# Performance work log

Measured on AMD Instinct MI355X. Metric: run time of the kernel, lower is better.

The kernel has to match this reference:

```python
import jax, jax.numpy as jnp
import numpy as np

B, L = 32768, 2048
NG, GL = 4, 64  # n_groups (bag channels), group length (MIL feature dim)


def _wn(v, g):
    # weight_norm: w = g * v / ||v|| (norm over in_ch, kernel dims per out channel)
    nrm = jnp.sqrt(jnp.sum(v * v, axis=(1, 2), keepdims=True))
    return g[:, None, None] * v / nrm


def _conv1d(x, w, b):
    # x: (N, C, L), w: (O, I, K), padding=1, stride=1
    out = jax.lax.conv_general_dilated(
        x, w, window_strides=(1,), padding=[(1, 1)],
        dimension_numbers=('NCH', 'OIH', 'NCH'))
    return out + b[None, :, None]


def setup_inputs() -> dict:
    key = jax.random.key(0)
    ks = jax.random.split(key, 12)
    x = jax.random.normal(ks[0], (B, L, 1), dtype=jnp.float32)
    index_all = jax.random.randint(ks[1], (NG, GL), 0, L)
    # conv1 (1 -> 1, k=3) with weight_norm params
    v1 = 0.01 * jax.random.normal(ks[2], (1, 1, 3), dtype=jnp.float32)
    g1 = jnp.ones((1,), dtype=jnp.float32)
    b1 = jnp.zeros((1,), dtype=jnp.float32)
    # conv2 (4 -> 4, k=3) with weight_norm params
    v2 = 0.01 * jax.random.normal(ks[3], (NG, NG, 3), dtype=jnp.float32)
    g2 = jnp.ones((NG,), dtype=jnp.float32)
    b2 = jnp.zeros((NG,), dtype=jnp.float32)
    # IMILmask linears (64 -> 64)
    sc = 1.0 / np.sqrt(GL)
    W1 = sc * jax.random.normal(ks[4], (GL, GL), dtype=jnp.float32)
    bl1 = jnp.zeros((GL,), dtype=jnp.float32)
    W2 = sc * jax.random.normal(ks[5], (GL, GL), dtype=jnp.float32)
    bl2 = jnp.zeros((GL,), dtype=jnp.float32)
    Wa = sc * jax.random.normal(ks[6], (GL, GL), dtype=jnp.float32)
    ba = jnp.zeros((GL,), dtype=jnp.float32)
    return {"x": x, "index_all": index_all, "v1": v1, "g1": g1, "b1": b1,
            "v2": v2, "g2": g2, "b2": b2, "W1": W1, "bl1": bl1,
            "W2": W2, "bl2": bl2, "Wa": Wa, "ba": ba}


def reference(x, index_all, v1, g1, b1, v2, g2, b2, W1, bl1, W2, bl2, Wa, ba):
    xp = jnp.transpose(x, (0, 2, 1))  # (B, 1, L)
    # site branch: conv -> tanh (in net) -> tanh again (forward applies tanh1 twice)
    w1 = _wn(v1, g1)
    x_site = jnp.tanh(jnp.tanh(_conv1d(xp, w1, b1)))  # (B, 1, L)
    # mapping_converge: ragged gather into bags; original detaches x here
    xg = jax.lax.stop_gradient(xp)[:, 0, :]           # (B, L)
    xm = xg[:, index_all]                             # (B, NG, GL)
    # IMILmask
    l1 = jax.nn.relu(xm @ W1.T + bl1)
    l2 = jax.nn.relu(xm @ W2.T + bl2)
    A = jax.nn.sigmoid((l1 + l2) @ Wa.T + ba)
    xmask = (A + 1.0) * xm                            # (B, NG, GL)
    # bag branch conv (channels = NG, length = GL)
    w2 = _wn(v2, g2)
    x_bag = jnp.tanh(jnp.tanh(_conv1d(xmask, w2, b2)))
    return (x_bag, x_site)
```

## Files before the change

kernel.cpp:

```cpp
#include <hip/hip_runtime.h>
#include <cmath>

#define BATCH 32768
#define LEN   2048
#define NGRP  4
#define GLEN  64

__device__ __forceinline__ float fast_tanh(float x){
    float ax = fabsf(x);
    float e  = __expf(-2.f*ax);
    float r  = __fdividef(1.f - e, 1.f + e);
    return copysignf(r, x);
}
__device__ __forceinline__ float tanh2(float x){ return fast_tanh(fast_tanh(x)); }

__global__ __launch_bounds__(256) void k_site(
    const float* __restrict__ x, const int* __restrict__ idx,
    const float* __restrict__ v1, const float* __restrict__ g1, const float* __restrict__ b1,
    float* __restrict__ xsite, float* __restrict__ xmws, int use_ws)
{
    float nrm = sqrtf(v1[0]*v1[0] + v1[1]*v1[1] + v1[2]*v1[2]);
    float s  = g1[0]/nrm;
    float w0 = v1[0]*s, w1 = v1[1]*s, w2 = v1[2]*s, bb = b1[0];

    __shared__ int sidx[256];
    sidx[threadIdx.x] = idx[threadIdx.x];
    __syncthreads();

    const int t = threadIdx.x;
    for (int rr = 0; rr < 4; ++rr){
        const int row = blockIdx.x*4 + rr;
        const float* xr  = x     + (size_t)row*LEN;
        float*       orr = xsite + (size_t)row*LEN;
        const int p0 = t*8;
        float4 a = *(const float4*)(xr + p0);
        float4 b = *(const float4*)(xr + p0 + 4);
        if (use_ws)
            xmws[(size_t)row*256 + t] = xr[sidx[t]];
        float in[10];
        in[0] = (p0 == 0) ? 0.f : xr[p0-1];
        in[1]=a.x; in[2]=a.y; in[3]=a.z; in[4]=a.w;
        in[5]=b.x; in[6]=b.y; in[7]=b.z; in[8]=b.w;
        in[9] = (p0 + 8 >= LEN) ? 0.f : xr[p0+8];
        float o[8];
        #pragma unroll
        for (int c = 0; c < 8; ++c)
            o[c] = tanh2(fmaf(w0, in[c], fmaf(w1, in[c+1], fmaf(w2, in[c+2], bb))));
        *(float4*)(orr + p0)     = make_float4(o[0],o[1],o[2],o[3]);
        *(float4*)(orr + p0 + 4) = make_float4(o[4],o[5],o[6],o[7]);
    }
}

__global__ __launch_bounds__(128) void k_bag(
    const float* __restrict__ x, const float* __restrict__ xmws, const int* __restrict__ idx,
    const float* __restrict__ v2, const float* __restrict__ g2, const float* __restrict__ b2,
    const float* __restrict__ W1, const float* __restrict__ bl1,
    const float* __restrict__ W2, const float* __restrict__ bl2,
    const float* __restrict__ Wa, const float* __restrict__ ba,
    float* __restrict__ xbag, int use_ws)
{
    const int lane = threadIdx.x & 63;
    const int wave = threadIdx.x >> 6;
    const int rl   = lane >> 2;
    const int g    = lane & 3;
    const int row  = blockIdx.x*32 + wave*16 + rl;

    float xm[GLEN];
    if (use_ws){
        const float4* p = (const float4*)(xmws + (size_t)row*256 + g*64);
        #pragma unroll
        for (int q = 0; q < 16; ++q){
            float4 v = p[q];
            xm[4*q+0]=v.x; xm[4*q+1]=v.y; xm[4*q+2]=v.z; xm[4*q+3]=v.w;
        }
    } else {
        const float* xr = x + (size_t)row*LEN;
        #pragma unroll
        for (int k = 0; k < GLEN; ++k) xm[k] = xr[idx[g*64 + k]];
    }

    float l12[GLEN];
    const float4* W1v = (const float4*)W1;
    const float4* W2v = (const float4*)W2;
    #pragma unroll 2
    for (int j = 0; j < GLEN; ++j){
        float a1 = bl1[j], a2 = bl2[j];
        #pragma unroll
        for (int q = 0; q < 16; ++q){
            float4 u = W1v[j*16 + q];
            float4 w = W2v[j*16 + q];
            a1 = fmaf(xm[4*q+0],u.x, fmaf(xm[4*q+1],u.y, fmaf(xm[4*q+2],u.z, fmaf(xm[4*q+3],u.w, a1))));
            a2 = fmaf(xm[4*q+0],w.x, fmaf(xm[4*q+1],w.y, fmaf(xm[4*q+2],w.z, fmaf(xm[4*q+3],w.w, a2))));
        }
        l12[j] = fmaxf(a1, 0.f) + fmaxf(a2, 0.f);
    }

    const float4* Wav = (const float4*)Wa;
    #pragma unroll 2
    for (int j = 0; j < GLEN; ++j){
        float a = ba[j];
        #pragma unroll
        for (int q = 0; q < 16; ++q){
            float4 u = Wav[j*16 + q];
            a = fmaf(l12[4*q+0],u.x, fmaf(l12[4*q+1],u.y, fmaf(l12[4*q+2],u.z, fmaf(l12[4*q+3],u.w, a))));
        }
        float A = __fdividef(1.f, 1.f + __expf(-a));
        xm[j] = (A + 1.f) * xm[j];
    }

    __shared__ float X[2*16*260];
    float* Xw = X + wave*(16*260) + rl*260 + g*65;
    #pragma unroll
    for (int k = 0; k < GLEN; ++k) Xw[k] = xm[k];
    __syncthreads();

    float wv[NGRP][3];
    float nn = 0.f;
    #pragma unroll
    for (int i = 0; i < NGRP; ++i)
        #pragma unroll
        for (int d = 0; d < 3; ++d){ float tv = v2[(g*NGRP + i)*3 + d]; nn += tv*tv; }
    float sc = g2[g] / sqrtf(nn);
    #pragma unroll
    for (int i = 0; i < NGRP; ++i)
        #pragma unroll
        for (int d = 0; d < 3; ++d) wv[i][d] = v2[(g*NGRP + i)*3 + d] * sc;

    float acc[GLEN];
    const float bo = b2[g];
    #pragma unroll
    for (int j = 0; j < GLEN; ++j) acc[j] = bo;
    const float* Xr = X + wave*(16*260) + rl*260;
    #pragma unroll
    for (int i = 0; i < NGRP; ++i){
        const float* c = Xr + i*65;
        float xp_ = 0.f, xc = c[0];
        #pragma unroll
        for (int j = 0; j < GLEN; ++j){
            float xn = (j < GLEN-1) ? c[j+1] : 0.f;
            acc[j] = fmaf(wv[i][0], xp_, fmaf(wv[i][1], xc, fmaf(wv[i][2], xn, acc[j])));
            xp_ = xc; xc = xn;
        }
    }

    float* ob = xbag + ((size_t)row*NGRP + g)*GLEN;
    #pragma unroll
    for (int q = 0; q < 16; ++q){
        float4 v = make_float4(tanh2(acc[4*q+0]), tanh2(acc[4*q+1]),
                               tanh2(acc[4*q+2]), tanh2(acc[4*q+3]));
        *(float4*)(ob + 4*q) = v;
    }
}

extern "C" void kernel_launch(void* const* d_in, const int* in_sizes, int n_in,
                              void* d_out, int out_size, void* d_ws, size_t ws_size,
                              hipStream_t stream) {
    const float* x   = (const float*)d_in[0];
    const int*   idx = (const int*)  d_in[1];
    const float* v1  = (const float*)d_in[2];
    const float* g1  = (const float*)d_in[3];
    const float* b1  = (const float*)d_in[4];
    const float* v2  = (const float*)d_in[5];
    const float* g2  = (const float*)d_in[6];
    const float* b2  = (const float*)d_in[7];
    const float* W1  = (const float*)d_in[8];
    const float* bl1 = (const float*)d_in[9];
    const float* W2  = (const float*)d_in[10];
    const float* bl2 = (const float*)d_in[11];
    const float* Wa  = (const float*)d_in[12];
    const float* ba  = (const float*)d_in[13];

    float* xbag  = (float*)d_out;
    float* xsite = (float*)d_out + (size_t)BATCH*NGRP*GLEN;
    float* xmws  = (float*)d_ws;
    const int use_ws = (ws_size >= (size_t)BATCH*256*sizeof(float)) ? 1 : 0;

    k_site<<<BATCH/4, 256, 0, stream>>>(x, idx, v1, g1, b1, xsite, xmws, use_ws);
    k_bag <<<BATCH/32, 128, 0, stream>>>(x, xmws, idx, v2, g2, b2,
                                         W1, bl1, W2, bl2, Wa, ba, xbag, use_ws);
}
```

Measured before the change: 710.6 us.

## Split bag MLP outputs across four threads per group via shared memory staging

k_bag now uses 256 threads per block, with four threads per (row, group). Each thread computes 16 of the 64 output features for the two linears, the attention layer and the conv, and intermediates are exchanged through padded shared memory. Results are staged in LDS so the final xbag store is contiguous and coalesced per block. The aim is to cut the per-thread register arrays of 64 floats, raise occupancy and coalesce the output. The cost is more syncthreads, more LDS traffic, and each thread still loading the full 64-element xm row, so that read is duplicated four times.

```diff
diff --git a/kernel.cpp b/kernel.cpp
--- a/kernel.cpp
+++ b/kernel.cpp
@@ -51,7 +51,7 @@
     }
 }
 
-__global__ __launch_bounds__(128) void k_bag(
+__global__ __launch_bounds__(256, 4) void k_bag(
     const float* __restrict__ x, const float* __restrict__ xmws, const int* __restrict__ idx,
     const float* __restrict__ v2, const float* __restrict__ g2, const float* __restrict__ b2,
     const float* __restrict__ W1, const float* __restrict__ bl1,
@@ -59,15 +59,20 @@
     const float* __restrict__ Wa, const float* __restrict__ ba,
     float* __restrict__ xbag, int use_ws)
 {
-    const int lane = threadIdx.x & 63;
-    const int wave = threadIdx.x >> 6;
-    const int rl   = lane >> 2;
-    const int g    = lane & 3;
-    const int row  = blockIdx.x*32 + wave*16 + rl;
+    const int t  = threadIdx.x;
+    const int s  = t & 3;
+    const int g  = (t >> 2) & 3;
+    const int rl = t >> 4;
+    const int row = blockIdx.x*16 + rl;
+    const int rg  = (rl << 2) | g;
+    const int j0  = s << 4;
+
+    __shared__ float b1s[64*65];
+    __shared__ float b2s[64*65];
 
     float xm[GLEN];
     if (use_ws){
-        const float4* p = (const float4*)(xmws + (size_t)row*256 + g*64);
+        const float4* p = (const float4*)(xmws + (size_t)row*256 + (g << 6));
         #pragma unroll
         for (int q = 0; q < 16; ++q){
             float4 v = p[q];
@@ -76,79 +81,113 @@
     } else {
         const float* xr = x + (size_t)row*LEN;
         #pragma unroll
-        for (int k = 0; k < GLEN; ++k) xm[k] = xr[idx[g*64 + k]];
-    }
-
-    float l12[GLEN];
-    const float4* W1v = (const float4*)W1;
-    const float4* W2v = (const float4*)W2;
-    #pragma unroll 2
-    for (int j = 0; j < GLEN; ++j){
-        float a1 = bl1[j], a2 = bl2[j];
-        #pragma unroll
+        for (int k = 0; k < GLEN; ++k) xm[k] = xr[idx[(g << 6) + k]];
+    }
+
+    {
+        const float4* W1v = (const float4*)W1;
+        const float4* W2v = (const float4*)W2;
+        float* Lw = b1s + rg*65 + j0;
+        #pragma unroll 2
+        for (int jj = 0; jj < 16; ++jj){
+            const int j = j0 + jj;
+            float a1 = bl1[j], a2 = bl2[j];
+            #pragma unroll
+            for (int q = 0; q < 16; ++q){
+                float4 u = W1v[j*16 + q];
+                float4 w = W2v[j*16 + q];
+                a1 = fmaf(xm[4*q+0],u.x, fmaf(xm[4*q+1],u.y, fmaf(xm[4*q+2],u.z, fmaf(xm[4*q+3],u.w, a1))));
+                a2 = fmaf(xm[4*q+0],w.x, fmaf(xm[4*q+1],w.y, fmaf(xm[4*q+2],w.z, fmaf(xm[4*q+3],w.w, a2))));
+            }
+            Lw[jj] = fmaxf(a1, 0.f) + fmaxf(a2, 0.f);
+        }
+    }
+    __syncthreads();
+
+    float acc[16];
+    #pragma unroll
+    for (int jj = 0; jj < 16; ++jj) acc[jj] = ba[j0 + jj];
+    {
+        const float4* Wav = (const float4*)Wa;
+        const float* Lr = b1s + rg*65;
+        #pragma unroll 2
         for (int q = 0; q < 16; ++q){
-            float4 u = W1v[j*16 + q];
-            float4 w = W2v[j*16 + q];
-            a1 = fmaf(xm[4*q+0],u.x, fmaf(xm[4*q+1],u.y, fmaf(xm[4*q+2],u.z, fmaf(xm[4*q+3],u.w, a1))));
-            a2 = fmaf(xm[4*q+0],w.x, fmaf(xm[4*q+1],w.y, fmaf(xm[4*q+2],w.z, fmaf(xm[4*q+3],w.w, a2))));
-        }
-        l12[j] = fmaxf(a1, 0.f) + fmaxf(a2, 0.f);
-    }
-
-    const float4* Wav = (const float4*)Wa;
-    #pragma unroll 2
-    for (int j = 0; j < GLEN; ++j){
-        float a = ba[j];
-        #pragma unroll
-        for (int q = 0; q < 16; ++q){
-            float4 u = Wav[j*16 + q];
-            a = fmaf(l12[4*q+0],u.x, fmaf(l12[4*q+1],u.y, fmaf(l12[4*q+2],u.z, fmaf(l12[4*q+3],u.w, a))));
-        }
-        float A = __fdividef(1.f, 1.f + __expf(-a));
-        xm[j] = (A + 1.f) * xm[j];
-    }
-
-    __shared__ float X[2*16*260];
-    float* Xw = X + wave*(16*260) + rl*260 + g*65;
-    #pragma unroll
-    for (int k = 0; k < GLEN; ++k) Xw[k] = xm[k];
-    __syncthreads();
-
-    float wv[NGRP][3];
-    float nn = 0.f;
-    #pragma unroll
-    for (int i = 0; i < NGRP; ++i)
-        #pragma unroll
-        for (int d = 0; d < 3; ++d){ float tv = v2[(g*NGRP + i)*3 + d]; nn += tv*tv; }
-    float sc = g2[g] / sqrtf(nn);
-    #pragma unroll
-    for (int i = 0; i < NGRP; ++i)
-        #pragma unroll
-        for (int d = 0; d < 3; ++d) wv[i][d] = v2[(g*NGRP + i)*3 + d] * sc;
-
-    float acc[GLEN];
-    const float bo = b2[g];
-    #pragma unroll
-    for (int j = 0; j < GLEN; ++j) acc[j] = bo;
-    const float* Xr = X + wave*(16*260) + rl*260;
-    #pragma unroll
-    for (int i = 0; i < NGRP; ++i){
-        const float* c = Xr + i*65;
-        float xp_ = 0.f, xc = c[0];
-        #pragma unroll
-        for (int j = 0; j < GLEN; ++j){
-            float xn = (j < GLEN-1) ? c[j+1] : 0.f;
-            acc[j] = fmaf(wv[i][0], xp_, fmaf(wv[i][1], xc, fmaf(wv[i][2], xn, acc[j])));
-            xp_ = xc; xc = xn;
-        }
-    }
-
-    float* ob = xbag + ((size_t)row*NGRP + g)*GLEN;
-    #pragma unroll
-    for (int q = 0; q < 16; ++q){
-        float4 v = make_float4(tanh2(acc[4*q+0]), tanh2(acc[4*q+1]),
-                               tanh2(acc[4*q+2]), tanh2(acc[4*q+3]));
-        *(float4*)(ob + 4*q) = v;
+            const float l0 = Lr[4*q+0], l1 = Lr[4*q+1], l2 = Lr[4*q+2], l3 = Lr[4*q+3];
+            #pragma unroll
+            for (int jj = 0; jj < 16; ++jj){
+                float4 u = Wav[(j0+jj)*16 + q];
+                acc[jj] = fmaf(l0,u.x, fmaf(l1,u.y, fmaf(l2,u.z, fmaf(l3,u.w, acc[jj]))));
+            }
+        }
+    }
+
+    {
+        float xs[16];
+        if (use_ws){
+            const float4* p = (const float4*)(xmws + (size_t)row*256 + (g << 6) + j0);
+            #pragma unroll
+            for (int c = 0; c < 4; ++c){
+                float4 v = p[c];
+                xs[4*c+0]=v.x; xs[4*c+1]=v.y; xs[4*c+2]=v.z; xs[4*c+3]=v.w;
+            }
+        } else {
+            const float* xr = x + (size_t)row*LEN;
+            #pragma unroll
+            for (int k = 0; k < 16; ++k) xs[k] = xr[idx[(g << 6) + j0 + k]];
+        }
+        float* Xw = b2s + rg*65 + j0;
+        #pragma unroll
+        for (int jj = 0; jj < 16; ++jj){
+            float A = __fdividef(1.f, 1.f + __expf(-acc[jj]));
+            Xw[jj] = (A + 1.f) * xs[jj];
+        }
+    }
+    __syncthreads();
+
+    {
+        float nn = 0.f;
+        #pragma unroll
+        for (int i = 0; i < NGRP; ++i)
+            #pragma unroll
+            for (int d = 0; d < 3; ++d){ float tv = v2[(g*NGRP + i)*3 + d]; nn += tv*tv; }
+        const float sc = g2[g] / sqrtf(nn);
+
+        float o[16];
+        const float bo = b2[g];
+        #pragma unroll
+        for (int jj = 0; jj < 16; ++jj) o[jj] = bo;
+
+        #pragma unroll
+        for (int i = 0; i < NGRP; ++i){
+            const float w0 = v2[(g*NGRP + i)*3 + 0] * sc;
+            const float w1 = v2[(g*NGRP + i)*3 + 1] * sc;
+            const float w2 = v2[(g*NGRP + i)*3 + 2] * sc;
+            const float* c = b2s + (((rl << 2) | i))*65 + j0;
+            float xp = (s == 0) ? 0.f : c[-1];
+            float xc = c[0];
+            #pragma unroll
+            for (int jj = 0; jj < 16; ++jj){
+                float xn = (jj < 15) ? c[jj+1] : ((s == 3) ? 0.f : c[16]);
+                o[jj] = fmaf(w0, xp, fmaf(w1, xc, fmaf(w2, xn, o[jj])));
+                xp = xc; xc = xn;
+            }
+        }
+        float* Ow = b1s + rg*65 + j0;
+        #pragma unroll
+        for (int jj = 0; jj < 16; ++jj) Ow[jj] = tanh2(o[jj]);
+    }
+    __syncthreads();
+
+    {
+        float* ob = xbag + (size_t)blockIdx.x * 4096;
+        const int r  = t >> 2;
+        const int cb = (t & 3) << 4;
+        const float* Or = b1s + r*65 + cb;
+        #pragma unroll
+        for (int c = 0; c < 4; ++c){
+            float4 v = make_float4(Or[4*c+0], Or[4*c+1], Or[4*c+2], Or[4*c+3]);
+            *(float4*)(ob + t*16 + 4*c) = v;
+        }
     }
 }
 
@@ -176,6 +215,6 @@
     const int use_ws = (ws_size >= (size_t)BATCH*256*sizeof(float)) ? 1 : 0;
 
     k_site<<<BATCH/4, 256, 0, stream>>>(x, idx, v1, g1, b1, xsite, xmws, use_ws);
-    k_bag <<<BATCH/32, 128, 0, stream>>>(x, xmws, idx, v2, g2, b2,
+    k_bag <<<BATCH/16, 256, 0, stream>>>(x, xmws, idx, v2, g2, b2,
                                          W1, bl1, W2, bl2, Wa, ba, xbag, use_ws);
 }
```

Result: slower. 1.362 ms (+91.7%).

## Cut k_bag register pressure by streaming conv output and fusing mask store

Applied to the files above, without the earlier changes.

Restructures k_bag to lower live register count. The masked features are written straight to shared memory instead of overwriting xm and copying it afterwards. The bag conv is reordered to loop over output position outermost with per-channel sliding windows, so the 64-entry acc array goes away and outputs are stored as float4 as they are produced. It also adds a min-blocks-per-CU hint to launch_bounds and fully unrolls the matmul loops; the larger code and any register cap could cause spills.

```diff
diff --git a/kernel.cpp b/kernel.cpp
--- a/kernel.cpp
+++ b/kernel.cpp
@@ -51,7 +51,7 @@
     }
 }
 
-__global__ __launch_bounds__(128) void k_bag(
+__global__ __launch_bounds__(128, 2) void k_bag(
     const float* __restrict__ x, const float* __restrict__ xmws, const int* __restrict__ idx,
     const float* __restrict__ v2, const float* __restrict__ g2, const float* __restrict__ b2,
     const float* __restrict__ W1, const float* __restrict__ bl1,
@@ -67,7 +67,7 @@
 
     float xm[GLEN];
     if (use_ws){
-        const float4* p = (const float4*)(xmws + (size_t)row*256 + g*64);
+        const float4* p = (const float4*)(xmws + (size_t)row*256 + (g << 6));
         #pragma unroll
         for (int q = 0; q < 16; ++q){
             float4 v = p[q];
@@ -76,79 +76,79 @@
     } else {
         const float* xr = x + (size_t)row*LEN;
         #pragma unroll
-        for (int k = 0; k < GLEN; ++k) xm[k] = xr[idx[g*64 + k]];
+        for (int k = 0; k < GLEN; ++k) xm[k] = xr[idx[(g << 6) + k]];
     }
 
     float l12[GLEN];
-    const float4* W1v = (const float4*)W1;
-    const float4* W2v = (const float4*)W2;
-    #pragma unroll 2
-    for (int j = 0; j < GLEN; ++j){
-        float a1 = bl1[j], a2 = bl2[j];
+    {
+        const float4* W1v = (const float4*)W1;
+        const float4* W2v = (const float4*)W2;
         #pragma unroll
-        for (int q = 0; q < 16; ++q){
-            float4 u = W1v[j*16 + q];
-            float4 w = W2v[j*16 + q];
-            a1 = fmaf(xm[4*q+0],u.x, fmaf(xm[4*q+1],u.y, fmaf(xm[4*q+2],u.z, fmaf(xm[4*q+3],u.w, a1))));
-            a2 = fmaf(xm[4*q+0],w.x, fmaf(xm[4*q+1],w.y, fmaf(xm[4*q+2],w.z, fmaf(xm[4*q+3],w.w, a2))));
+        for (int j = 0; j < GLEN; ++j){
+            float a1 = bl1[j], a2 = bl2[j];
+            #pragma unroll
+            for (int q = 0; q < 16; ++q){
+                float4 u = W1v[j*16 + q];
+                float4 w = W2v[j*16 + q];
+                a1 = fmaf(xm[4*q+0],u.x, fmaf(xm[4*q+1],u.y, fmaf(xm[4*q+2],u.z, fmaf(xm[4*q+3],u.w, a1))));
+                a2 = fmaf(xm[4*q+0],w.x, fmaf(xm[4*q+1],w.y, fmaf(xm[4*q+2],w.z, fmaf(xm[4*q+3],w.w, a2))));
+            }
+            l12[j] = fmaxf(a1, 0.f) + fmaxf(a2, 0.f);
         }
-        l12[j] = fmaxf(a1, 0.f) + fmaxf(a2, 0.f);
-    }
-
-    const float4* Wav = (const float4*)Wa;
-    #pragma unroll 2
-    for (int j = 0; j < GLEN; ++j){
-        float a = ba[j];
-        #pragma unroll
-        for (int q = 0; q < 16; ++q){
-            float4 u = Wav[j*16 + q];
-            a = fmaf(l12[4*q+0],u.x, fmaf(l12[4*q+1],u.y, fmaf(l12[4*q+2],u.z, fmaf(l12[4*q+3],u.w, a))));
-        }
-        float A = __fdividef(1.f, 1.f + __expf(-a));
-        xm[j] = (A + 1.f) * xm[j];
     }
 
     __shared__ float X[2*16*260];
-    float* Xw = X + wave*(16*260) + rl*260 + g*65;
-    #pragma unroll
-    for (int k = 0; k < GLEN; ++k) Xw[k] = xm[k];
+    {
+        float* Xw = X + wave*(16*260) + rl*260 + g*65;
+        const float4* Wav = (const float4*)Wa;
+        #pragma unroll
+        for (int j = 0; j < GLEN; ++j){
+            float a = ba[j];
+            #pragma unroll
+            for (int q = 0; q < 16; ++q){
+                float4 u = Wav[j*16 + q];
+                a = fmaf(l12[4*q+0],u.x, fmaf(l12[4*q+1],u.y, fmaf(l12[4*q+2],u.z, fmaf(l12[4*q+3],u.w, a))));
+            }
+            float A = __fdividef(1.f, 1.f + __expf(-a));
+            Xw[j] = (A + 1.f) * xm[j];
+        }
+    }
     __syncthreads();
 
-    float wv[NGRP][3];
-    float nn = 0.f;
-    #pragma unroll
-    for (int i = 0; i < NGRP; ++i)
+    {
+        float nn = 0.f;
         #pragma unroll
-        for (int d = 0; d < 3; ++d){ float tv = v2[(g*NGRP + i)*3 + d]; nn += tv*tv; }
-    float sc = g2[g] / sqrtf(nn);
-    #pragma unroll
-    for (int i = 0; i < NGRP; ++i)
+        for (int i = 0; i < NGRP; ++i)
+            #pragma unroll
+            for (int d = 0; d < 3; ++d){ float tv = v2[(g*NGRP + i)*3 + d]; nn += tv*tv; }
+        const float sc = g2[g] / sqrtf(nn);
+        float wv[NGRP][3];
         #pragma unroll
-        for (int d = 0; d < 3; ++d) wv[i][d] = v2[(g*NGRP + i)*3 + d] * sc;
+        for (int i = 0; i < NGRP; ++i)
+            #pragma unroll
+            for (int d = 0; d < 3; ++d) wv[i][d] = v2[(g*NGRP + i)*3 + d] * sc;
 
-    float acc[GLEN];
-    const float bo = b2[g];
-    #pragma unroll
-    for (int j = 0; j < GLEN; ++j) acc[j] = bo;
-    const float* Xr = X + wave*(16*260) + rl*260;
-    #pragma unroll
-    for (int i = 0; i < NGRP; ++i){
-        const float* c = Xr + i*65;
-        float xp_ = 0.f, xc = c[0];
+        const float* Xr = X + wave*(16*260) + rl*260;
+        const float bo = b2[g];
+        float xp[NGRP], xc[NGRP];
+        #pragma unroll
+        for (int i = 0; i < NGRP; ++i){ xp[i] = 0.f; xc[i] = Xr[i*65]; }
+
+        float* ob = xbag + (size_t)row*(NGRP*GLEN) + (g << 6);
+        float o4[4];
         #pragma unroll
         for (int j = 0; j < GLEN; ++j){
-            float xn = (j < GLEN-1) ? c[j+1] : 0.f;
-            acc[j] = fmaf(wv[i][0], xp_, fmaf(wv[i][1], xc, fmaf(wv[i][2], xn, acc[j])));
-            xp_ = xc; xc = xn;
+            float o = bo;
+            #pragma unroll
+            for (int i = 0; i < NGRP; ++i){
+                float xn = (j < GLEN-1) ? Xr[i*65 + j + 1] : 0.f;
+                o = fmaf(wv[i][0], xp[i], fmaf(wv[i][1], xc[i], fmaf(wv[i][2], xn, o)));
+                xp[i] = xc[i]; xc[i] = xn;
+            }
+            o4[j & 3] = tanh2(o);
+            if ((j & 3) == 3)
+                *(float4*)(ob + (j & ~3)) = make_float4(o4[0], o4[1], o4[2], o4[3]);
         }
-    }
-
-    float* ob = xbag + ((size_t)row*NGRP + g)*GLEN;
-    #pragma unroll
-    for (int q = 0; q < 16; ++q){
-        float4 v = make_float4(tanh2(acc[4*q+0]), tanh2(acc[4*q+1]),
-                               tanh2(acc[4*q+2]), tanh2(acc[4*q+3]));
-        *(float4*)(ob + 4*q) = v;
     }
 }
 
```

After: 687.1 us. -3.3%, faster.
